# Kernel tuning notes

Measured on AMD Instinct MI355X. Metric: run time of the kernel, lower is better.

Reference implementation:

```python
import jax, jax.numpy as jnp
import numpy as np

EPS = 1e-6
NUM_HEADS = 16

def _favor_positive_features(x):
    # softmax-style normalized positive features along last dim
    p = jnp.exp(x - jnp.max(x, axis=-1, keepdims=True))
    return p / (jnp.sum(p, axis=-1, keepdims=True) + EPS)

def setup_inputs() -> dict:
    key = jax.random.key(0)
    ks = jax.random.split(key, 9)
    B, L, D = 2, 2048, 1024
    s = 0.02
    return {
        "hidden_states": jax.random.normal(ks[0], (B, L, D), dtype=jnp.float32),
        # Linear weights stored as [in, out] (y = x @ W + b), matching torch Linear math
        "Wq": jax.random.normal(ks[1], (D, D), dtype=jnp.float32) * s,
        "bq": jnp.zeros((D,), dtype=jnp.float32),
        "Wk": jax.random.normal(ks[2], (D, D), dtype=jnp.float32) * s,
        "bk": jnp.zeros((D,), dtype=jnp.float32),
        "Wv": jax.random.normal(ks[3], (D, D), dtype=jnp.float32) * s,
        "bv": jnp.zeros((D,), dtype=jnp.float32),
        "Wo": jax.random.normal(ks[4], (D, D), dtype=jnp.float32) * s,
        "bo": jnp.zeros((D,), dtype=jnp.float32),
    }

def reference(hidden_states, Wq, bq, Wk, bk, Wv, bv, Wo, bo):
    B, L, D = hidden_states.shape
    H = NUM_HEADS
    hd = D // H

    def split_heads(x):  # [B,L,D] -> [B,H,L,hd]
        return x.reshape(B, L, H, hd).transpose(0, 2, 1, 3)

    q = split_heads(hidden_states @ Wq + bq)
    k = split_heads(hidden_states @ Wk + bk)
    v = split_heads(hidden_states @ Wv + bv)

    q = _favor_positive_features(q)
    k = _favor_positive_features(k)

    # quadratic scores as in the original module
    numerator = jnp.einsum('bhld,bhmd->bhlm', q, k)
    # einsum(q, ones) over d == sum_d q, broadcast over m (identical math)
    denominator = jnp.sum(q, axis=-1, keepdims=True)  # [B,H,L,1]
    attention_probs = numerator / (denominator + EPS)
    # dropout prob = 0.0 -> identity
    context = jnp.einsum('bhlm,bhmd->bhld', attention_probs, v)
    context = context.transpose(0, 2, 1, 3).reshape(B, L, D)
    return context @ Wo + bo
```

## Files before the change

### kernel.cpp

```cpp
#include <hip/hip_runtime.h>


#define EPSV 1e-6f
#define MDIM 4096
#define DDIM 1024
#define HEADS 16
#define HD 64

typedef __attribute__((ext_vector_type(8))) short short8;
typedef __attribute__((ext_vector_type(4))) float f32x4;

__device__ inline ushort f2bf(float x) {
    unsigned int b = __float_as_uint(x);
    unsigned int r = (b + 0x7FFFu + ((b >> 16) & 1u)) >> 16;
    return (ushort)r;
}
__device__ inline float bf2f(ushort u) { return __uint_as_float(((unsigned int)u) << 16); }

__device__ inline void gld_lds16(const ushort* g, ushort* l) {
    __builtin_amdgcn_global_load_lds(
        (const __attribute__((address_space(1))) unsigned int*)g,
        (__attribute__((address_space(3))) unsigned int*)l, 16, 0, 0);
}

__global__ __launch_bounds__(256) void split_kernel(const float* __restrict__ x,
                                                    ushort* __restrict__ hi,
                                                    ushort* __restrict__ lo)
{
    const int i = (blockIdx.x * 256 + threadIdx.x) * 4;
    const float4 v = *(const float4*)&x[i];
    ushort4 h, l;
    h.x = f2bf(v.x); l.x = f2bf(v.x - bf2f(h.x));
    h.y = f2bf(v.y); l.y = f2bf(v.y - bf2f(h.y));
    h.z = f2bf(v.z); l.z = f2bf(v.z - bf2f(h.z));
    h.w = f2bf(v.w); l.w = f2bf(v.w - bf2f(h.w));
    *(ushort4*)&hi[i] = h;
    *(ushort4*)&lo[i] = l;
}

__global__ __launch_bounds__(256) void wsplit_kernel(
    const float* __restrict__ W0, const float* __restrict__ W1,
    const float* __restrict__ W2, const float* __restrict__ W3,
    ushort* __restrict__ T0h, ushort* __restrict__ T0l,
    ushort* __restrict__ T1h, ushort* __restrict__ T1l,
    ushort* __restrict__ T2h, ushort* __restrict__ T2l,
    ushort* __restrict__ T3h, ushort* __restrict__ T3l)
{
    const float* W; ushort* Th; ushort* Tl;
    if (blockIdx.z == 0)      { W = W0; Th = T0h; Tl = T0l; }
    else if (blockIdx.z == 1) { W = W1; Th = T1h; Tl = T1l; }
    else if (blockIdx.z == 2) { W = W2; Th = T2h; Tl = T2l; }
    else                      { W = W3; Th = T3h; Tl = T3l; }

    __shared__ float t[32][33];
    const int tt = threadIdx.x;
    const int r = tt >> 3, c4 = (tt & 7) * 4;
    const int k0 = blockIdx.x * 32, n0 = blockIdx.y * 32;

    const float4 v = *(const float4*)&W[(size_t)(k0 + r) * DDIM + n0 + c4];
    t[r][c4 + 0] = v.x; t[r][c4 + 1] = v.y; t[r][c4 + 2] = v.z; t[r][c4 + 3] = v.w;
    __syncthreads();

    const float x0 = t[c4 + 0][r], x1 = t[c4 + 1][r], x2 = t[c4 + 2][r], x3 = t[c4 + 3][r];
    ushort4 h, l;
    h.x = f2bf(x0); l.x = f2bf(x0 - bf2f(h.x));
    h.y = f2bf(x1); l.y = f2bf(x1 - bf2f(h.y));
    h.z = f2bf(x2); l.z = f2bf(x2 - bf2f(h.z));
    h.w = f2bf(x3); l.w = f2bf(x3 - bf2f(h.w));
    *(ushort4*)&Th[(size_t)(n0 + r) * DDIM + k0 + c4] = h;
    *(ushort4*)&Tl[(size_t)(n0 + r) * DDIM + k0 + c4] = l;
}

__global__ __launch_bounds__(256, 2) void gemm_mfma(
    const ushort* __restrict__ Ahi, const ushort* __restrict__ Alo,
    const ushort* __restrict__ B0h, const ushort* __restrict__ B0l,
    const ushort* __restrict__ B1h, const ushort* __restrict__ B1l,
    const ushort* __restrict__ B2h, const ushort* __restrict__ B2l,
    const float* __restrict__ bias0, const float* __restrict__ bias1, const float* __restrict__ bias2,
    float* __restrict__ C0, float* __restrict__ C1, float* __restrict__ C2)
{
    const ushort* Bh; const ushort* Bl; const float* bias; float* C;
    if (blockIdx.z == 0)      { Bh = B0h; Bl = B0l; bias = bias0; C = C0; }
    else if (blockIdx.z == 1) { Bh = B1h; Bl = B1l; bias = bias1; C = C1; }
    else                      { Bh = B2h; Bl = B2l; bias = bias2; C = C2; }

    __shared__ __align__(16) ushort lds[4][8][512];

    const int tid = threadIdx.x;
    const int w = tid >> 6, l = tid & 63;
    const int row0 = blockIdx.x * 128, col0 = blockIdx.y * 128;
    const int wr = w >> 1, wc = w & 1;

    const ushort* gs; int outer0;
    if (w == 0)      { gs = Ahi; outer0 = row0; }
    else if (w == 1) { gs = Alo; outer0 = row0; }
    else if (w == 2) { gs = Bh;  outer0 = col0; }
    else             { gs = Bl;  outer0 = col0; }
    const size_t lanebase = (size_t)(outer0 + (l & 15)) * DDIM + ((l >> 4) * 8);

    f32x4 acc[4][4];
    #pragma unroll
    for (int i = 0; i < 4; ++i)
        #pragma unroll
        for (int j = 0; j < 4; ++j) acc[i][j] = (f32x4){0.f, 0.f, 0.f, 0.f};

    for (int kc = 0; kc < DDIM; kc += 32) {
        __syncthreads();
        #pragma unroll
        for (int f = 0; f < 8; ++f)
            gld_lds16(gs + lanebase + (size_t)f * 16 * DDIM + kc, &lds[w][f][0]);
        __syncthreads();

        short8 ah[4], al[4], bh[4], bl[4];
        #pragma unroll
        for (int i = 0; i < 4; ++i) {
            ah[i] = *(const short8*)&lds[0][wr * 4 + i][l * 8];
            al[i] = *(const short8*)&lds[1][wr * 4 + i][l * 8];
            bh[i] = *(const short8*)&lds[2][wc * 4 + i][l * 8];
            bl[i] = *(const short8*)&lds[3][wc * 4 + i][l * 8];
        }
        #pragma unroll
        for (int i = 0; i < 4; ++i)
            #pragma unroll
            for (int j = 0; j < 4; ++j) {
                acc[i][j] = __builtin_amdgcn_mfma_f32_16x16x32_bf16(ah[i], bh[j], acc[i][j], 0, 0, 0);
                acc[i][j] = __builtin_amdgcn_mfma_f32_16x16x32_bf16(ah[i], bl[j], acc[i][j], 0, 0, 0);
                acc[i][j] = __builtin_amdgcn_mfma_f32_16x16x32_bf16(al[i], bh[j], acc[i][j], 0, 0, 0);
            }
    }

    #pragma unroll
    for (int j = 0; j < 4; ++j) {
        const int col = col0 + (wc * 4 + j) * 16 + (l & 15);
        const float bb = bias[col];
        #pragma unroll
        for (int i = 0; i < 4; ++i) {
            const int rbase = row0 + (wr * 4 + i) * 16 + (l >> 4) * 4;
            #pragma unroll
            for (int q = 0; q < 4; ++q)
                C[(size_t)(rbase + q) * DDIM + col] = acc[i][j][q] + bb;
        }
    }
}

__global__ __launch_bounds__(256) void feature_kernel(float* __restrict__ buf,
                                                      float* __restrict__ den)
{
    const int wid  = blockIdx.x * 4 + (threadIdx.x >> 6);
    const int lane = threadIdx.x & 63;
    const int row = wid >> 4;
    const int h   = wid & 15;
    float* p = buf + (size_t)row * DDIM + h * HD;

    const float v = p[lane];
    float m = v;
    #pragma unroll
    for (int o = 32; o; o >>= 1) m = fmaxf(m, __shfl_xor(m, o, 64));
    const float e = expf(v - m);
    float s = e;
    #pragma unroll
    for (int o = 32; o; o >>= 1) s += __shfl_xor(s, o, 64);
    const float q = e / (s + EPSV);
    p[lane] = q;
    if (den != nullptr) {
        float d = q;
        #pragma unroll
        for (int o = 32; o; o >>= 1) d += __shfl_xor(d, o, 64);
        if (lane == 0) den[wid] = d;
    }
}

#define MSUB 32
__global__ __launch_bounds__(256) void kv_partial_kernel(
    const float* __restrict__ Kf, const float* __restrict__ V, float* __restrict__ KVp)
{
    const int z = blockIdx.x;
    const int chunk = z & 7;
    const int bh = z >> 3;
    const int h = bh & 15;
    const int b = bh >> 4;

    __shared__ float Ks[MSUB][HD];
    __shared__ float Vs[MSUB][HD];

    const int t = threadIdx.x;
    const int d0 = (t >> 4) * 4;
    const int e0 = (t & 15) * 4;
    float acc[4][4];
    #pragma unroll
    for (int i = 0; i < 4; ++i)
        #pragma unroll
        for (int j = 0; j < 4; ++j) acc[i][j] = 0.f;

    const int base_tok = b * 2048 + chunk * 256;
    for (int sc = 0; sc < 8; ++sc) {
        __syncthreads();
        #pragma unroll
        for (int u = 0; u < 2; ++u) {
            const int f = t + u * 256;
            const int tok = f >> 4;
            const int c4 = (f & 15) * 4;
            const size_t g = (size_t)(base_tok + sc * MSUB + tok) * DDIM + h * HD + c4;
            *(float4*)&Ks[tok][c4] = *(const float4*)&Kf[g];
            *(float4*)&Vs[tok][c4] = *(const float4*)&V[g];
        }
        __syncthreads();
        #pragma unroll
        for (int mm = 0; mm < MSUB; ++mm) {
            const float4 k4 = *(const float4*)&Ks[mm][d0];
            const float4 v4 = *(const float4*)&Vs[mm][e0];
            const float kr[4] = {k4.x, k4.y, k4.z, k4.w};
            const float vr[4] = {v4.x, v4.y, v4.z, v4.w};
            #pragma unroll
            for (int i = 0; i < 4; ++i)
                #pragma unroll
                for (int j = 0; j < 4; ++j)
                    acc[i][j] = fmaf(kr[i], vr[j], acc[i][j]);
        }
    }
    float* outp = KVp + (size_t)z * 4096;
    #pragma unroll
    for (int i = 0; i < 4; ++i)
        *(float4*)&outp[(d0 + i) * HD + e0] =
            make_float4(acc[i][0], acc[i][1], acc[i][2], acc[i][3]);
}

__global__ __launch_bounds__(256) void kv_reduce_kernel(const float* __restrict__ KVp,
                                                        float* __restrict__ KV)
{
    const int idx = blockIdx.x * 256 + threadIdx.x;
    const int bh = idx >> 12;
    const int off = idx & 4095;
    float s = 0.f;
    #pragma unroll
    for (int c = 0; c < 8; ++c) s += KVp[(size_t)(bh * 8 + c) * 4096 + off];
    KV[idx] = s;
}

__global__ __launch_bounds__(256) void context_kernel(
    const float* __restrict__ QF, const float* __restrict__ KV, const float* __restrict__ den,
    ushort* __restrict__ Chi, ushort* __restrict__ Clo)
{
    const int z = blockIdx.x;
    const int tc = z & 31;
    const int bh = z >> 5;
    const int h = bh & 15;
    const int b = bh >> 4;

    __shared__ float KVs[HD][HD];
    const int t = threadIdx.x;
    #pragma unroll
    for (int u = 0; u < 4; ++u) {
        const int f = t + u * 256;
        *(float4*)&KVs[0][f * 4] = *(const float4*)&KV[(size_t)bh * 4096 + f * 4];
    }
    __syncthreads();

    const int wave = t >> 6;
    const int lane = t & 63;
    for (int it = 0; it < 16; ++it) {
        const int tok = tc * 64 + it * 4 + wave;
        const int row = b * 2048 + tok;
        const size_t idx = (size_t)row * DDIM + h * HD + lane;
        const float qv = QF[idx];
        float acc = 0.f;
        #pragma unroll
        for (int e = 0; e < 64; ++e) {
            const float qe = __shfl(qv, e, 64);
            acc = fmaf(qe, KVs[e][lane], acc);
        }
        const float r = acc / (den[row * HEADS + h] + EPSV);
        const ushort hh = f2bf(r);
        Chi[idx] = hh;
        Clo[idx] = f2bf(r - bf2f(hh));
    }
}

extern "C" void kernel_launch(void* const* d_in, const int* in_sizes, int n_in,
                              void* d_out, int out_size, void* d_ws, size_t ws_size,
                              hipStream_t stream)
{
    const float* X  = (const float*)d_in[0];
    const float* Wq = (const float*)d_in[1];
    const float* bq = (const float*)d_in[2];
    const float* Wk = (const float*)d_in[3];
    const float* bk = (const float*)d_in[4];
    const float* Wv = (const float*)d_in[5];
    const float* bv = (const float*)d_in[6];
    const float* Wo = (const float*)d_in[7];
    const float* bo = (const float*)d_in[8];
    float* out = (float*)d_out;

    float* ws  = (float*)d_ws;
    float* Q   = ws;
    float* Kb  = ws + 4194304;
    float* Vb  = ws + 8388608;
    float* den = ws + 12582912;
    float* KV  = den + 65536;
    float* KVp = KV + 131072;
    ushort* Xhi = (ushort*)(KVp + 1048576);
    ushort* Xlo = Xhi + 4194304;
    ushort* Wqh = Xlo + 4194304;
    ushort* Wql = Wqh + 1048576;
    ushort* Wkh = Wql + 1048576;
    ushort* Wkl = Wkh + 1048576;
    ushort* Wvh = Wkl + 1048576;
    ushort* Wvl = Wvh + 1048576;
    ushort* Woh = Wvl + 1048576;
    ushort* Wol = Woh + 1048576;
    ushort* Chi = Xhi;
    ushort* Clo = Xlo;

    split_kernel<<<4096, 256, 0, stream>>>(X, Xhi, Xlo);
    wsplit_kernel<<<dim3(32, 32, 4), 256, 0, stream>>>(
        Wq, Wk, Wv, Wo, Wqh, Wql, Wkh, Wkl, Wvh, Wvl, Woh, Wol);

    gemm_mfma<<<dim3(32, 8, 3), 256, 0, stream>>>(
        Xhi, Xlo, Wqh, Wql, Wkh, Wkl, Wvh, Wvl, bq, bk, bv, Q, Kb, Vb);

    feature_kernel<<<16384, 256, 0, stream>>>(Q, den);
    feature_kernel<<<16384, 256, 0, stream>>>(Kb, nullptr);

    kv_partial_kernel<<<256, 256, 0, stream>>>(Kb, Vb, KVp);
    kv_reduce_kernel<<<512, 256, 0, stream>>>(KVp, KV);

    context_kernel<<<1024, 256, 0, stream>>>(Q, KV, den, Chi, Clo);

    gemm_mfma<<<dim3(32, 8, 1), 256, 0, stream>>>(
        Chi, Clo, Woh, Wol, Woh, Wol, Woh, Wol, bo, bo, bo, out, out, out);
}
```

Before: 349.9 us.

## Switch split-bf16 GEMMs to fp16 activations with scaled two-term fp16 weights

Replaces the three-MFMA bf16 hi/lo emulation with fp16: activations become a single fp16 copy and weights are split into an fp16 hi plus a lo residual scaled by 256, so each tile needs two MFMAs instead of three. The A lo buffer and its loads disappear, and the residual is accumulated separately and rescaled in the epilogue. The output GEMM now uses a narrower column tile (WJ=2) to launch more blocks. The catch is precision: activations are rounded to fp16, which has a narrower range and fewer mantissa bits than the old roughly 16-bit emulation.

```diff
diff --git a/kernel.cpp b/kernel.cpp
--- a/kernel.cpp
+++ b/kernel.cpp
@@ -7,46 +7,37 @@
 #define HEADS 16
 #define HD 64
 
-typedef __attribute__((ext_vector_type(8))) short short8;
+typedef __attribute__((ext_vector_type(8))) _Float16 half8;
+typedef __attribute__((ext_vector_type(4))) _Float16 half4;
 typedef __attribute__((ext_vector_type(4))) float f32x4;
 
-__device__ inline ushort f2bf(float x) {
-    unsigned int b = __float_as_uint(x);
-    unsigned int r = (b + 0x7FFFu + ((b >> 16) & 1u)) >> 16;
-    return (ushort)r;
-}
-__device__ inline float bf2f(ushort u) { return __uint_as_float(((unsigned int)u) << 16); }
-
-__device__ inline void gld_lds16(const ushort* g, ushort* l) {
+__device__ inline void gld_lds16(const _Float16* g, _Float16* l) {
     __builtin_amdgcn_global_load_lds(
         (const __attribute__((address_space(1))) unsigned int*)g,
         (__attribute__((address_space(3))) unsigned int*)l, 16, 0, 0);
 }
 
-__global__ __launch_bounds__(256) void split_kernel(const float* __restrict__ x,
-                                                    ushort* __restrict__ hi,
-                                                    ushort* __restrict__ lo)
-{
-    const int i = (blockIdx.x * 256 + threadIdx.x) * 4;
-    const float4 v = *(const float4*)&x[i];
-    ushort4 h, l;
-    h.x = f2bf(v.x); l.x = f2bf(v.x - bf2f(h.x));
-    h.y = f2bf(v.y); l.y = f2bf(v.y - bf2f(h.y));
-    h.z = f2bf(v.z); l.z = f2bf(v.z - bf2f(h.z));
-    h.w = f2bf(v.w); l.w = f2bf(v.w - bf2f(h.w));
-    *(ushort4*)&hi[i] = h;
-    *(ushort4*)&lo[i] = l;
+__global__ __launch_bounds__(256) void xhalf_kernel(const float* __restrict__ x,
+                                                    _Float16* __restrict__ xh)
+{
+    const int i = (blockIdx.x * 256 + threadIdx.x) * 8;
+    const float4 v0 = *(const float4*)&x[i];
+    const float4 v1 = *(const float4*)&x[i + 4];
+    half8 h;
+    h[0] = (_Float16)v0.x; h[1] = (_Float16)v0.y; h[2] = (_Float16)v0.z; h[3] = (_Float16)v0.w;
+    h[4] = (_Float16)v1.x; h[5] = (_Float16)v1.y; h[6] = (_Float16)v1.z; h[7] = (_Float16)v1.w;
+    *(half8*)&xh[i] = h;
 }
 
 __global__ __launch_bounds__(256) void wsplit_kernel(
     const float* __restrict__ W0, const float* __restrict__ W1,
     const float* __restrict__ W2, const float* __restrict__ W3,
-    ushort* __restrict__ T0h, ushort* __restrict__ T0l,
-    ushort* __restrict__ T1h, ushort* __restrict__ T1l,
-    ushort* __restrict__ T2h, ushort* __restrict__ T2l,
-    ushort* __restrict__ T3h, ushort* __restrict__ T3l)
-{
-    const float* W; ushort* Th; ushort* Tl;
+    _Float16* __restrict__ T0h, _Float16* __restrict__ T0l,
+    _Float16* __restrict__ T1h, _Float16* __restrict__ T1l,
+    _Float16* __restrict__ T2h, _Float16* __restrict__ T2l,
+    _Float16* __restrict__ T3h, _Float16* __restrict__ T3l)
+{
+    const float* W; _Float16* Th; _Float16* Tl;
     if (blockIdx.z == 0)      { W = W0; Th = T0h; Tl = T0l; }
     else if (blockIdx.z == 1) { W = W1; Th = T1h; Tl = T1l; }
     else if (blockIdx.z == 2) { W = W2; Th = T2h; Tl = T2l; }
@@ -62,83 +53,95 @@
     __syncthreads();
 
     const float x0 = t[c4 + 0][r], x1 = t[c4 + 1][r], x2 = t[c4 + 2][r], x3 = t[c4 + 3][r];
-    ushort4 h, l;
-    h.x = f2bf(x0); l.x = f2bf(x0 - bf2f(h.x));
-    h.y = f2bf(x1); l.y = f2bf(x1 - bf2f(h.y));
-    h.z = f2bf(x2); l.z = f2bf(x2 - bf2f(h.z));
-    h.w = f2bf(x3); l.w = f2bf(x3 - bf2f(h.w));
-    *(ushort4*)&Th[(size_t)(n0 + r) * DDIM + k0 + c4] = h;
-    *(ushort4*)&Tl[(size_t)(n0 + r) * DDIM + k0 + c4] = l;
-}
-
+    half4 h, l;
+    h[0] = (_Float16)x0; l[0] = (_Float16)((x0 - (float)h[0]) * 256.0f);
+    h[1] = (_Float16)x1; l[1] = (_Float16)((x1 - (float)h[1]) * 256.0f);
+    h[2] = (_Float16)x2; l[2] = (_Float16)((x2 - (float)h[2]) * 256.0f);
+    h[3] = (_Float16)x3; l[3] = (_Float16)((x3 - (float)h[3]) * 256.0f);
+    *(half4*)&Th[(size_t)(n0 + r) * DDIM + k0 + c4] = h;
+    *(half4*)&Tl[(size_t)(n0 + r) * DDIM + k0 + c4] = l;
+}
+
+template<int WJ>
 __global__ __launch_bounds__(256, 2) void gemm_mfma(
-    const ushort* __restrict__ Ahi, const ushort* __restrict__ Alo,
-    const ushort* __restrict__ B0h, const ushort* __restrict__ B0l,
-    const ushort* __restrict__ B1h, const ushort* __restrict__ B1l,
-    const ushort* __restrict__ B2h, const ushort* __restrict__ B2l,
+    const _Float16* __restrict__ A,
+    const _Float16* __restrict__ B0h, const _Float16* __restrict__ B0l,
+    const _Float16* __restrict__ B1h, const _Float16* __restrict__ B1l,
+    const _Float16* __restrict__ B2h, const _Float16* __restrict__ B2l,
     const float* __restrict__ bias0, const float* __restrict__ bias1, const float* __restrict__ bias2,
     float* __restrict__ C0, float* __restrict__ C1, float* __restrict__ C2)
 {
-    const ushort* Bh; const ushort* Bl; const float* bias; float* C;
+    const _Float16* Bh; const _Float16* Bl; const float* bias; float* C;
     if (blockIdx.z == 0)      { Bh = B0h; Bl = B0l; bias = bias0; C = C0; }
     else if (blockIdx.z == 1) { Bh = B1h; Bl = B1l; bias = bias1; C = C1; }
     else                      { Bh = B2h; Bl = B2l; bias = bias2; C = C2; }
 
-    __shared__ __align__(16) ushort lds[4][8][512];
+    constexpr int FA = 8;
+    constexpr int FB = 2 * WJ;
+    constexpr int NF = FA + 2 * FB;
+    constexpr int FPW = NF / 4;
+
+    __shared__ __align__(16) _Float16 lds[NF * 512];
 
     const int tid = threadIdx.x;
     const int w = tid >> 6, l = tid & 63;
-    const int row0 = blockIdx.x * 128, col0 = blockIdx.y * 128;
+    const int row0 = blockIdx.x * 128, col0 = blockIdx.y * (32 * WJ);
     const int wr = w >> 1, wc = w & 1;
 
-    const ushort* gs; int outer0;
-    if (w == 0)      { gs = Ahi; outer0 = row0; }
-    else if (w == 1) { gs = Alo; outer0 = row0; }
-    else if (w == 2) { gs = Bh;  outer0 = col0; }
-    else             { gs = Bl;  outer0 = col0; }
-    const size_t lanebase = (size_t)(outer0 + (l & 15)) * DDIM + ((l >> 4) * 8);
-
-    f32x4 acc[4][4];
+    const int lrow = (l & 15);
+    const int lk   = (l >> 4) * 8;
+
+    f32x4 acc1[4][WJ], acc2[4][WJ];
     #pragma unroll
     for (int i = 0; i < 4; ++i)
         #pragma unroll
-        for (int j = 0; j < 4; ++j) acc[i][j] = (f32x4){0.f, 0.f, 0.f, 0.f};
+        for (int j = 0; j < WJ; ++j) {
+            acc1[i][j] = (f32x4){0.f, 0.f, 0.f, 0.f};
+            acc2[i][j] = (f32x4){0.f, 0.f, 0.f, 0.f};
+        }
 
     for (int kc = 0; kc < DDIM; kc += 32) {
         __syncthreads();
         #pragma unroll
-        for (int f = 0; f < 8; ++f)
-            gld_lds16(gs + lanebase + (size_t)f * 16 * DDIM + kc, &lds[w][f][0]);
+        for (int u = 0; u < FPW; ++u) {
+            const int g = w * FPW + u;
+            const _Float16* src; int outer;
+            if (g < FA)           { src = A;  outer = row0 + g * 16; }
+            else if (g < FA + FB) { src = Bh; outer = col0 + (g - FA) * 16; }
+            else                  { src = Bl; outer = col0 + (g - FA - FB) * 16; }
+            gld_lds16(src + (size_t)(outer + lrow) * DDIM + kc + lk, &lds[g * 512]);
+        }
         __syncthreads();
 
-        short8 ah[4], al[4], bh[4], bl[4];
-        #pragma unroll
-        for (int i = 0; i < 4; ++i) {
-            ah[i] = *(const short8*)&lds[0][wr * 4 + i][l * 8];
-            al[i] = *(const short8*)&lds[1][wr * 4 + i][l * 8];
-            bh[i] = *(const short8*)&lds[2][wc * 4 + i][l * 8];
-            bl[i] = *(const short8*)&lds[3][wc * 4 + i][l * 8];
+        half8 a[4], bh[WJ], bl[WJ];
+        #pragma unroll
+        for (int i = 0; i < 4; ++i)
+            a[i] = *(const half8*)&lds[(wr * 4 + i) * 512 + l * 8];
+        #pragma unroll
+        for (int j = 0; j < WJ; ++j) {
+            bh[j] = *(const half8*)&lds[(FA + wc * WJ + j) * 512 + l * 8];
+            bl[j] = *(const half8*)&lds[(FA + FB + wc * WJ + j) * 512 + l * 8];
         }
         #pragma unroll
         for (int i = 0; i < 4; ++i)
             #pragma unroll
-            for (int j = 0; j < 4; ++j) {
-                acc[i][j] = __builtin_amdgcn_mfma_f32_16x16x32_bf16(ah[i], bh[j], acc[i][j], 0, 0, 0);
-                acc[i][j] = __builtin_amdgcn_mfma_f32_16x16x32_bf16(ah[i], bl[j], acc[i][j], 0, 0, 0);
-                acc[i][j] = __builtin_amdgcn_mfma_f32_16x16x32_bf16(al[i], bh[j], acc[i][j], 0, 0, 0);
+            for (int j = 0; j < WJ; ++j) {
+                acc1[i][j] = __builtin_amdgcn_mfma_f32_16x16x32_f16(a[i], bh[j], acc1[i][j], 0, 0, 0);
+                acc2[i][j] = __builtin_amdgcn_mfma_f32_16x16x32_f16(a[i], bl[j], acc2[i][j], 0, 0, 0);
             }
     }
 
     #pragma unroll
-    for (int j = 0; j < 4; ++j) {
-        const int col = col0 + (wc * 4 + j) * 16 + (l & 15);
+    for (int j = 0; j < WJ; ++j) {
+        const int col = col0 + (wc * WJ + j) * 16 + lrow;
         const float bb = bias[col];
         #pragma unroll
         for (int i = 0; i < 4; ++i) {
             const int rbase = row0 + (wr * 4 + i) * 16 + (l >> 4) * 4;
             #pragma unroll
             for (int q = 0; q < 4; ++q)
-                C[(size_t)(rbase + q) * DDIM + col] = acc[i][j][q] + bb;
+                C[(size_t)(rbase + q) * DDIM + col] =
+                    acc1[i][j][q] + acc2[i][j][q] * 0.00390625f + bb;
         }
     }
 }
@@ -239,7 +242,7 @@
 
 __global__ __launch_bounds__(256) void context_kernel(
     const float* __restrict__ QF, const float* __restrict__ KV, const float* __restrict__ den,
-    ushort* __restrict__ Chi, ushort* __restrict__ Clo)
+    _Float16* __restrict__ Ch)
 {
     const int z = blockIdx.x;
     const int tc = z & 31;
@@ -270,9 +273,7 @@
             acc = fmaf(qe, KVs[e][lane], acc);
         }
         const float r = acc / (den[row * HEADS + h] + EPSV);
-        const ushort hh = f2bf(r);
-        Chi[idx] = hh;
-        Clo[idx] = f2bf(r - bf2f(hh));
+        Ch[idx] = (_Float16)r;
     }
 }
 
@@ -298,25 +299,23 @@
     float* den = ws + 12582912;
     float* KV  = den + 65536;
     float* KVp = KV + 131072;
-    ushort* Xhi = (ushort*)(KVp + 1048576);
-    ushort* Xlo = Xhi + 4194304;
-    ushort* Wqh = Xlo + 4194304;
-    ushort* Wql = Wqh + 1048576;
-    ushort* Wkh = Wql + 1048576;
-    ushort* Wkl = Wkh + 1048576;
-    ushort* Wvh = Wkl + 1048576;
-    ushort* Wvl = Wvh + 1048576;
-    ushort* Woh = Wvl + 1048576;
-    ushort* Wol = Woh + 1048576;
-    ushort* Chi = Xhi;
-    ushort* Clo = Xlo;
-
-    split_kernel<<<4096, 256, 0, stream>>>(X, Xhi, Xlo);
+    _Float16* Xh  = (_Float16*)(KVp + 1048576);
+    _Float16* Wqh = Xh + 4194304;
+    _Float16* Wql = Wqh + 1048576;
+    _Float16* Wkh = Wql + 1048576;
+    _Float16* Wkl = Wkh + 1048576;
+    _Float16* Wvh = Wkl + 1048576;
+    _Float16* Wvl = Wvh + 1048576;
+    _Float16* Woh = Wvl + 1048576;
+    _Float16* Wol = Woh + 1048576;
+    _Float16* Ch  = Xh;
+
+    xhalf_kernel<<<2048, 256, 0, stream>>>(X, Xh);
     wsplit_kernel<<<dim3(32, 32, 4), 256, 0, stream>>>(
         Wq, Wk, Wv, Wo, Wqh, Wql, Wkh, Wkl, Wvh, Wvl, Woh, Wol);
 
-    gemm_mfma<<<dim3(32, 8, 3), 256, 0, stream>>>(
-        Xhi, Xlo, Wqh, Wql, Wkh, Wkl, Wvh, Wvl, bq, bk, bv, Q, Kb, Vb);
+    gemm_mfma<4><<<dim3(32, 8, 3), 256, 0, stream>>>(
+        Xh, Wqh, Wql, Wkh, Wkl, Wvh, Wvl, bq, bk, bv, Q, Kb, Vb);
 
     feature_kernel<<<16384, 256, 0, stream>>>(Q, den);
     feature_kernel<<<16384, 256, 0, stream>>>(Kb, nullptr);
@@ -324,8 +323,8 @@
     kv_partial_kernel<<<256, 256, 0, stream>>>(Kb, Vb, KVp);
     kv_reduce_kernel<<<512, 256, 0, stream>>>(KVp, KV);
 
-    context_kernel<<<1024, 256, 0, stream>>>(Q, KV, den, Chi, Clo);
-
-    gemm_mfma<<<dim3(32, 8, 1), 256, 0, stream>>>(
-        Chi, Clo, Woh, Wol, Woh, Wol, Woh, Wol, bo, bo, bo, out, out, out);
-}
+    context_kernel<<<1024, 256, 0, stream>>>(Q, KV, den, Ch);
+
+    gemm_mfma<2><<<dim3(32, 16, 1), 256, 0, stream>>>(
+        Ch, Woh, Wol, Woh, Wol, Woh, Wol, bo, bo, bo, out, out, out);
+}
```

After: 312.3 us. -10.7%, faster.
